# Kernel optimization log

Hardware: AMD Instinct MI355X
Metric: run time of the kernel (lower is better)

The kernel has to match this reference:

```python
import jax, jax.numpy as jnp
import numpy as np

H_HEADS = 8
DIM_HEAD = 64
NEG_BIAS = -1.0e9


def setup_inputs() -> dict:
    key = jax.random.key(0)
    ks = jax.random.split(key, 8)
    b, n, l = 4, 4096, 256
    qd, cd = 512, 768
    inner = H_HEADS * DIM_HEAD  # 512
    x = jax.random.normal(ks[0], (b, n, qd), dtype=jnp.float32)
    context = jax.random.normal(ks[1], (b, l, cd), dtype=jnp.float32)
    mask = jax.random.randint(ks[2], (b, l, 128, 128), 0, 2).astype(jnp.int32)
    Wq = jax.random.normal(ks[3], (qd, inner), dtype=jnp.float32) * 0.02
    Wk = jax.random.normal(ks[4], (cd, inner), dtype=jnp.float32) * 0.02
    Wv = jax.random.normal(ks[5], (cd, inner), dtype=jnp.float32) * 0.02
    Wo = jax.random.normal(ks[6], (inner, qd), dtype=jnp.float32) * 0.02
    bo = jnp.zeros((qd,), dtype=jnp.float32)
    return {"x": x, "context": context, "mask": mask,
            "Wq": Wq, "Wk": Wk, "Wv": Wv, "Wo": Wo, "bo": bo}


def _split_heads(t, h):
    # 'b n (h d) -> (b h) n d'
    b, n, hd = t.shape
    d = hd // h
    return t.reshape(b, n, h, d).transpose(0, 2, 1, 3).reshape(b * h, n, d)


def reference(x, context, mask, Wq, Wk, Wv, Wo, bo):
    h = H_HEADS
    scale = DIM_HEAD ** (-0.5)
    b, n, _ = x.shape
    l = context.shape[1]
    size = int(round(n ** 0.5))  # spatial side of the query grid

    q = _split_heads(x @ Wq, h)        # (b*h, n, d)
    k = _split_heads(context @ Wk, h)  # (b*h, l, d)
    v = _split_heads(context @ Wv, h)  # (b*h, l, d)

    sim = jnp.einsum('bid,bjd->bij', q, k) * scale  # (b*h, n, l)

    # F.interpolate(mask, size=size) with default 'nearest': idx = floor(i * H_in / size)
    Hin = mask.shape[2]
    idx = (jnp.arange(size) * Hin) // size
    m = mask[:, :, idx[:, None], idx[None, :]]       # (b, l, size, size)
    m = m.reshape(b, l, n).transpose(0, 2, 1)        # (b, n, l)
    m = jnp.tile(m, (h, 1, 1)).astype(bool)          # (b*h, n, l), tile order as in torch .tile(h,1,1)
    sim = jnp.where(m, sim, sim + NEG_BIAS)

    attn = jax.nn.softmax(sim, axis=-1)
    out = jnp.einsum('bij,bjd->bid', attn, v)        # (b*h, n, d)
    # '(b h) n d -> b n (h d)'
    out = out.reshape(b, h, n, DIM_HEAD).transpose(0, 2, 1, 3).reshape(b, n, h * DIM_HEAD)
    return out @ Wo + bo
```

## Files before the change

kernel.cpp:

```cpp
#include <hip/hip_runtime.h>
#include <hip/hip_bf16.h>

typedef __attribute__((ext_vector_type(8))) short short8;
typedef __attribute__((ext_vector_type(4))) float f32x4;

__device__ __forceinline__ unsigned short f2bf(float f) {
  unsigned int u = __float_as_uint(f);
  u = (u + 0x7FFFu + ((u >> 16) & 1u)) >> 16;
  return (unsigned short)u;
}

__device__ __forceinline__ unsigned int pk2(float a, float b) {
  __hip_bfloat162 h = __float22bfloat162_rn(make_float2(a, b));
  return *reinterpret_cast<unsigned int*>(&h);
}

__device__ __forceinline__ void gl_lds16(const void* g, void* l) {
  __builtin_amdgcn_global_load_lds(
      (const __attribute__((address_space(1))) void*)g,
      (__attribute__((address_space(3))) void*)l, 16, 0, 0);
}

__device__ __forceinline__ void fence_barrier() {
  asm volatile("" ::: "memory");
  __builtin_amdgcn_s_barrier();
  asm volatile("" ::: "memory");
}

__device__ __forceinline__ void store4_bf16(unsigned short* p, int stride,
                                            float v0, float v1, float v2, float v3) {
  unsigned int u01 = pk2(v0, v1), u23 = pk2(v2, v3);
  p[0] = (unsigned short)u01;
  p[stride] = (unsigned short)(u01 >> 16);
  p[2 * stride] = (unsigned short)u23;
  p[3 * stride] = (unsigned short)(u23 >> 16);
}

__global__ void prep_all(const float* __restrict__ Wq, const float* __restrict__ Wk,
                         const float* __restrict__ Wv, const float* __restrict__ Wo,
                         unsigned short* __restrict__ WqT, unsigned short* __restrict__ WkT,
                         unsigned short* __restrict__ WvT, unsigned short* __restrict__ WoT,
                         const int* __restrict__ mask, unsigned char* __restrict__ Mout,
                         const float* __restrict__ x, const float* __restrict__ ctx,
                         unsigned short* __restrict__ xb, unsigned short* __restrict__ ctxb) {
  __shared__ char smem[64 * 256];
  const int bid = blockIdx.x;
  if (bid >= 576) {
    int i = (bid - 576) * 256 + threadIdx.x;
    const float4* src;
    ushort4* dst;
    if (i < 2097152) {
      src = (const float4*)x + i;
      dst = (ushort4*)xb + i;
    } else {
      int j = i - 2097152;
      if (j >= 196608) return;
      src = (const float4*)ctx + j;
      dst = (ushort4*)ctxb + j;
    }
    float4 v = *src;
    ushort4 o;
    o.x = f2bf(v.x); o.y = f2bf(v.y); o.z = f2bf(v.z); o.w = f2bf(v.w);
    *dst = o;
    return;
  }
  if (bid < 320) {
    unsigned short(*t)[65] = (unsigned short(*)[65])smem;
    const float* W; unsigned short* WT; int K, rel;
    float scale = 1.f;
    if (bid < 64)       { W = Wq; WT = WqT; K = 512; rel = bid; scale = 0.125f * 1.4426950408889634f; }
    else if (bid < 160) { W = Wk; WT = WkT; K = 768; rel = bid - 64; }
    else if (bid < 256) { W = Wv; WT = WvT; K = 768; rel = bid - 160; }
    else                { W = Wo; WT = WoT; K = 512; rel = bid - 256; }
    const int N = 512;
    const int tk = rel >> 3, tn = rel & 7;
    const int k0 = tk * 64, n0 = tn * 64;
    const int tt = threadIdx.x;
#pragma unroll
    for (int e = 0; e < 16; ++e) {
      int idx = e * 256 + tt;
      int r = idx >> 6, c = idx & 63;
      t[r][c] = f2bf(scale * W[(size_t)(k0 + r) * N + n0 + c]);
    }
    __syncthreads();
#pragma unroll
    for (int e = 0; e < 16; ++e) {
      int idx = e * 256 + tt;
      int rr = idx & 63, cc = idx >> 6;
      WT[(size_t)(n0 + cc) * K + k0 + rr] = t[rr][cc];
    }
  } else {
    unsigned char* bits = (unsigned char*)smem;
    const int rel = bid - 320;
    const int r2g = rel & 63, bp = rel >> 6;
    const int j = threadIdx.x;
    const int4* row = (const int4*)(mask + ((size_t)(bp * 256 + j) * 128 + r2g * 2) * 128);
#pragma unroll 8
    for (int q = 0; q < 32; ++q) {
      int4 v = row[q];
      bits[(2 * q) * 256 + j] = v.x ? 1 : 0;
      bits[(2 * q + 1) * 256 + j] = v.z ? 1 : 0;
    }
    __syncthreads();
    const int t2 = threadIdx.x;
    const int c = t2 >> 2, ch = t2 & 3;
    uint4* dst = (uint4*)(Mout + ((size_t)bp * 4096 + r2g * 64 + c) * 256 + ch * 64);
#pragma unroll
    for (int q = 0; q < 4; ++q) {
      unsigned int wd[4];
#pragma unroll
      for (int wq = 0; wq < 4; ++wq) {
        unsigned int v = 0;
#pragma unroll
        for (int bb = 0; bb < 4; ++bb) {
          int ob = ch * 64 + q * 16 + wq * 4 + bb;
          int jj = ((ob & 15) << 4) | (ob >> 4);
          v |= ((unsigned int)bits[c * 256 + jj]) << (8 * bb);
        }
        wd[wq] = v;
      }
      uint4 vv; vv.x = wd[0]; vv.y = wd[1]; vv.z = wd[2]; vv.w = wd[3];
      dst[q] = vv;
    }
  }
}

__global__ __launch_bounds__(256, 2) void proj_all(
    const unsigned short* __restrict__ xb, const unsigned short* __restrict__ ctxb,
    const unsigned short* __restrict__ WqT, const unsigned short* __restrict__ WkT,
    const unsigned short* __restrict__ WvT,
    unsigned short* __restrict__ Qb, unsigned short* __restrict__ Kb,
    unsigned short* __restrict__ VTb) {
  __shared__ unsigned short lds_a[2][128 * 64];
  __shared__ unsigned short lds_b[2][128 * 64];
  const int tid = threadIdx.x;
  const int w = tid >> 6, lane = tid & 63;
  const int lo = lane & 15, hi = lane >> 4;
  const int wr = w >> 1, wc = w & 1;
  const int bid = blockIdx.x;
  const int wg = (bid & 7) * 96 + (bid >> 3);

  if (wg < 512) {
    const int m0 = (wg >> 2) * 128, n0 = (wg & 3) * 128;
    const int K = 512;
    f32x4 acc[4][4];
#pragma unroll
    for (int m = 0; m < 4; ++m)
#pragma unroll
      for (int n = 0; n < 4; ++n) acc[m][n] = (f32x4){0.f, 0.f, 0.f, 0.f};

    auto stage = [&](int buf, int k0) {
#pragma unroll
      for (int c = 0; c < 4; ++c) {
        int o = (tid + c * 256) * 16;
        int row = o >> 7, colb = (o & 127) ^ ((row & 7) << 4);
        gl_lds16((const char*)xb + ((size_t)(m0 + row) * K + k0) * 2 + colb,
                 (char*)lds_a[buf] + (w * 64 + c * 256) * 16);
      }
#pragma unroll
      for (int c = 0; c < 4; ++c) {
        int o = (tid + c * 256) * 16;
        int row = o >> 7, colb = (o & 127) ^ ((row & 7) << 4);
        gl_lds16((const char*)WqT + ((size_t)(n0 + row) * K + k0) * 2 + colb,
                 (char*)lds_b[buf] + (w * 64 + c * 256) * 16);
      }
    };

    stage(0, 0);
    int cur = 0;
    for (int t = 0; t < 8; ++t) {
      if (t < 7) {
        stage(cur ^ 1, (t + 1) * 64);
        asm volatile("s_waitcnt vmcnt(8)" ::: "memory");
      } else {
        asm volatile("s_waitcnt vmcnt(0)" ::: "memory");
      }
      fence_barrier();
      short8 a[2][4], b[2][4];
#pragma unroll
      for (int kk = 0; kk < 2; ++kk) {
#pragma unroll
        for (int m = 0; m < 4; ++m) {
          int row = wr * 64 + m * 16 + lo;
          a[kk][m] = *(const short8*)((const char*)lds_a[cur] + row * 128 +
                                      (((kk * 32 + hi * 8) * 2) ^ ((row & 7) << 4)));
        }
#pragma unroll
        for (int n = 0; n < 4; ++n) {
          int row = wc * 64 + n * 16 + lo;
          b[kk][n] = *(const short8*)((const char*)lds_b[cur] + row * 128 +
                                      (((kk * 32 + hi * 8) * 2) ^ ((row & 7) << 4)));
        }
      }
#pragma unroll
      for (int kk = 0; kk < 2; ++kk)
#pragma unroll
        for (int m = 0; m < 4; ++m)
#pragma unroll
          for (int n = 0; n < 4; ++n)
            acc[m][n] = __builtin_amdgcn_mfma_f32_16x16x32_bf16(a[kk][m], b[kk][n], acc[m][n], 0, 0, 0);
      if (t < 7) fence_barrier();
      cur ^= 1;
    }
#pragma unroll
    for (int m = 0; m < 4; ++m)
#pragma unroll
      for (int n = 0; n < 4; ++n) {
        int rbase = m0 + wr * 64 + m * 16 + hi * 4;
        int col = n0 + wc * 64 + n * 16 + lo;
        store4_bf16(&Qb[(size_t)rbase * 512 + col], 512,
                    acc[m][n][0], acc[m][n][1], acc[m][n][2], acc[m][n][3]);
      }
  } else {
    const int rel = wg - 512;
    const int z = rel >> 7, t5 = rel & 127;
    const unsigned short* BT = z ? WvT : WkT;
    const int m0 = (t5 >> 3) * 64, n0 = (t5 & 7) * 64;
    const int K = 768;
    f32x4 acc[2][2];
#pragma unroll
    for (int m = 0; m < 2; ++m)
#pragma unroll
      for (int n = 0; n < 2; ++n) acc[m][n] = (f32x4){0.f, 0.f, 0.f, 0.f};

    auto stage = [&](int buf, int k0) {
#pragma unroll
      for (int c = 0; c < 2; ++c) {
        int o = (tid + c * 256) * 16;
        int row = o >> 7, colb = (o & 127) ^ ((row & 7) << 4);
        gl_lds16((const char*)ctxb + ((size_t)(m0 + row) * K + k0) * 2 + colb,
                 (char*)lds_a[buf] + (w * 64 + c * 256) * 16);
        gl_lds16((const char*)BT + ((size_t)(n0 + row) * K + k0) * 2 + colb,
                 (char*)lds_b[buf] + (w * 64 + c * 256) * 16);
      }
    };

    stage(0, 0);
    int cur = 0;
    for (int t = 0; t < 12; ++t) {
      if (t < 11) {
        stage(cur ^ 1, (t + 1) * 64);
        asm volatile("s_waitcnt vmcnt(4)" ::: "memory");
      } else {
        asm volatile("s_waitcnt vmcnt(0)" ::: "memory");
      }
      fence_barrier();
      short8 a[2][2], b[2][2];
#pragma unroll
      for (int kk = 0; kk < 2; ++kk) {
#pragma unroll
        for (int m = 0; m < 2; ++m) {
          int row = wr * 32 + m * 16 + lo;
          a[kk][m] = *(const short8*)((const char*)lds_a[cur] + row * 128 +
                                      (((kk * 32 + hi * 8) * 2) ^ ((row & 7) << 4)));
        }
#pragma unroll
        for (int n = 0; n < 2; ++n) {
          int row = wc * 32 + n * 16 + lo;
          b[kk][n] = *(const short8*)((const char*)lds_b[cur] + row * 128 +
                                      (((kk * 32 + hi * 8) * 2) ^ ((row & 7) << 4)));
        }
      }
#pragma unroll
      for (int kk = 0; kk < 2; ++kk)
#pragma unroll
        for (int m = 0; m < 2; ++m)
#pragma unroll
          for (int n = 0; n < 2; ++n)
            acc[m][n] = __builtin_amdgcn_mfma_f32_16x16x32_bf16(a[kk][m], b[kk][n], acc[m][n], 0, 0, 0);
      if (t < 11) fence_barrier();
      cur ^= 1;
    }
#pragma unroll
    for (int m = 0; m < 2; ++m)
#pragma unroll
      for (int n = 0; n < 2; ++n) {
        int col = n0 + wc * 32 + n * 16 + lo;
        int rowg = m0 + wr * 32 + m * 16 + hi * 4;
        if (z == 0) {
          store4_bf16(&Kb[(size_t)rowg * 512 + col], 512,
                      acc[m][n][0], acc[m][n][1], acc[m][n][2], acc[m][n][3]);
        } else {
          unsigned int u01 = pk2(acc[m][n][0], acc[m][n][1]);
          unsigned int u23 = pk2(acc[m][n][2], acc[m][n][3]);
          uint2 vv; vv.x = u01; vv.y = u23;
          *(uint2*)&VTb[((size_t)(rowg >> 8) * 512 + col) * 256 + (rowg & 255)] = vv;
        }
      }
  }
}

__global__ void attn_kernel(const unsigned short* __restrict__ Qb,
                            const unsigned short* __restrict__ Kb,
                            const unsigned short* __restrict__ VTb,
                            const unsigned char* __restrict__ Mu8,
                            unsigned short* __restrict__ AOb) {
  __shared__ unsigned short kt[256 * 64];
  const int tid = threadIdx.x, w = tid >> 6, lane = tid & 63;
  const int lo = lane & 15, hi = lane >> 4;
  const int bid = blockIdx.x;
  const int wg = (bid & 7) * 256 + (bid >> 3);
  const int qt = wg & 63, h = (wg >> 6) & 7, b = wg >> 9;

#pragma unroll
  for (int c = 0; c < 8; ++c) {
    int o = (tid + c * 256) * 16;
    int j = o >> 7, colb = (o & 127) ^ ((j & 7) << 4);
    gl_lds16((const char*)Kb + ((size_t)((b * 256 + j) * 512 + h * 64)) * 2 + colb,
             (char*)kt + (w * 64 + c * 256) * 16);
  }
  short8 qf[2];
  {
    int qrow = qt * 64 + w * 16 + lo;
#pragma unroll
    for (int kk = 0; kk < 2; ++kk)
      qf[kk] = *(const short8*)&Qb[(size_t)(b * 4096 + qrow) * 512 + h * 64 + kk * 32 + hi * 8];
  }
  const unsigned char* mrow = Mu8 + ((size_t)(h & 3) * 4096 + qt * 64 + w * 16) * 256;
  uint4 mv[4];
#pragma unroll
  for (int r = 0; r < 4; ++r)
    mv[r] = *(const uint4*)(mrow + (hi * 4 + r) * 256 + lo * 16);
  __syncthreads();

  f32x4 acc[16];
#pragma unroll
  for (int nt = 0; nt < 16; ++nt) acc[nt] = (f32x4){0.f, 0.f, 0.f, 0.f};
  __builtin_amdgcn_s_setprio(1);
#pragma unroll
  for (int nt = 0; nt < 16; ++nt) {
    int j = nt * 16 + lo;
#pragma unroll
    for (int kk = 0; kk < 2; ++kk) {
      short8 bfr = *(const short8*)((const char*)kt + j * 128 +
                                    (((kk * 32 + hi * 8) * 2) ^ ((j & 7) << 4)));
      acc[nt] = __builtin_amdgcn_mfma_f32_16x16x32_bf16(qf[kk], bfr, acc[nt], 0, 0, 0);
    }
  }
  __builtin_amdgcn_s_setprio(0);

  float rsum[4] = {0.f, 0.f, 0.f, 0.f};
#pragma unroll
  for (int nt = 0; nt < 16; ++nt)
#pragma unroll
    for (int r = 0; r < 4; ++r) {
      unsigned int word = (nt < 4) ? mv[r].x : (nt < 8) ? mv[r].y : (nt < 12) ? mv[r].z : mv[r].w;
      unsigned int mbyte = (word >> ((nt & 3) * 8)) & 0xFFu;
      float p = exp2f(acc[nt][r]);
      p = mbyte ? p : 0.f;
      acc[nt][r] = p;
      rsum[r] += p;
    }
  float rinv[4];
#pragma unroll
  for (int r = 0; r < 4; ++r) {
#pragma unroll
    for (int m2 = 1; m2 < 16; m2 <<= 1)
      rsum[r] += __shfl_xor(rsum[r], m2, 64);
    rinv[r] = 1.f / rsum[r];
  }

  __syncthreads();

  {
    char* pl = (char*)kt;
    const int q0 = w * 16 + hi * 4;
    const int ro0 = (q0 + 0) * 512, sw0 = ((q0 + 0) & 7) << 4;
    const int ro1 = (q0 + 1) * 512, sw1 = ((q0 + 1) & 7) << 4;
    const int ro2 = (q0 + 2) * 512, sw2 = ((q0 + 2) & 7) << 4;
    const int ro3 = (q0 + 3) * 512, sw3 = ((q0 + 3) & 7) << 4;
#pragma unroll
    for (int nt = 0; nt < 16; ++nt) {
      int j2 = (nt * 16 + lo) * 2;
      unsigned int u01 = pk2(acc[nt][0] * rinv[0], acc[nt][1] * rinv[1]);
      unsigned int u23 = pk2(acc[nt][2] * rinv[2], acc[nt][3] * rinv[3]);
      *(unsigned short*)(pl + ro0 + (j2 ^ sw0)) = (unsigned short)u01;
      *(unsigned short*)(pl + ro1 + (j2 ^ sw1)) = (unsigned short)(u01 >> 16);
      *(unsigned short*)(pl + ro2 + (j2 ^ sw2)) = (unsigned short)u23;
      *(unsigned short*)(pl + ro3 + (j2 ^ sw3)) = (unsigned short)(u23 >> 16);
    }
  }
  __syncthreads();

  const int dh = w & 1, qh = w >> 1;
  f32x4 aco[2][2];
#pragma unroll
  for (int m = 0; m < 2; ++m)
#pragma unroll
    for (int n = 0; n < 2; ++n) aco[m][n] = (f32x4){0.f, 0.f, 0.f, 0.f};
  const size_t vbase = ((size_t)b * 512 + h * 64 + dh * 32) * 256;
#pragma unroll
  for (int ks = 0; ks < 8; ++ks) {
    short8 pa[2];
#pragma unroll
    for (int m = 0; m < 2; ++m) {
      int q = qh * 32 + m * 16 + lo;
      pa[m] = *(const short8*)((const char*)kt + q * 512 +
                               (((ks * 32 + hi * 8) * 2) ^ ((q & 7) << 4)));
    }
    __builtin_amdgcn_s_setprio(1);
#pragma unroll
    for (int n = 0; n < 2; ++n) {
      short8 vb = *(const short8*)&VTb[vbase + (size_t)(n * 16 + lo) * 256 + ks * 32 + hi * 8];
#pragma unroll
      for (int m = 0; m < 2; ++m)
        aco[m][n] = __builtin_amdgcn_mfma_f32_16x16x32_bf16(pa[m], vb, aco[m][n], 0, 0, 0);
    }
    __builtin_amdgcn_s_setprio(0);
  }

#pragma unroll
  for (int m = 0; m < 2; ++m) {
#pragma unroll
    for (int n = 0; n < 2; ++n) {
      int col = h * 64 + dh * 32 + n * 16 + lo;
      int rowg = qt * 64 + qh * 32 + m * 16 + hi * 4;
      store4_bf16(&AOb[(size_t)(b * 4096 + rowg) * 512 + col], 512,
                  aco[m][n][0], aco[m][n][1], aco[m][n][2], aco[m][n][3]);
    }
  }
}

__global__ __launch_bounds__(256, 2) void gemm_o(
    const unsigned short* __restrict__ A, const unsigned short* __restrict__ BT,
    float* __restrict__ Cout, const float* __restrict__ bias) {
  __shared__ unsigned short lds_a[2][128 * 64];
  __shared__ unsigned short lds_b[2][128 * 64];
  const int tid = threadIdx.x;
  const int w = tid >> 6, lane = tid & 63;
  const int lo = lane & 15, hi = lane >> 4;
  const int bid = blockIdx.x;
  const int wg = (bid & 7) * 64 + (bid >> 3);
  const int m0 = (wg >> 2) * 128, n0 = (wg & 3) * 128;
  const int wr = w >> 1, wc = w & 1;
  const int K = 512, N = 512;
  f32x4 acc[4][4];
#pragma unroll
  for (int m = 0; m < 4; ++m)
#pragma unroll
    for (int n = 0; n < 4; ++n) acc[m][n] = (f32x4){0.f, 0.f, 0.f, 0.f};

  auto stage = [&](int buf, int k0) {
#pragma unroll
    for (int c = 0; c < 4; ++c) {
      int o = (tid + c * 256) * 16;
      int row = o >> 7, colb = (o & 127) ^ ((row & 7) << 4);
      gl_lds16((const char*)A + ((size_t)(m0 + row) * K + k0) * 2 + colb,
               (char*)lds_a[buf] + (w * 64 + c * 256) * 16);
    }
#pragma unroll
    for (int c = 0; c < 4; ++c) {
      int o = (tid + c * 256) * 16;
      int row = o >> 7, colb = (o & 127) ^ ((row & 7) << 4);
      gl_lds16((const char*)BT + ((size_t)(n0 + row) * K + k0) * 2 + colb,
               (char*)lds_b[buf] + (w * 64 + c * 256) * 16);
    }
  };

  stage(0, 0);
  int cur = 0;
  for (int t = 0; t < 8; ++t) {
    if (t < 7) {
      stage(cur ^ 1, (t + 1) * 64);
      asm volatile("s_waitcnt vmcnt(8)" ::: "memory");
    } else {
      asm volatile("s_waitcnt vmcnt(0)" ::: "memory");
    }
    fence_barrier();
    short8 a[2][4], b[2][4];
#pragma unroll
    for (int kk = 0; kk < 2; ++kk) {
#pragma unroll
      for (int m = 0; m < 4; ++m) {
        int row = wr * 64 + m * 16 + lo;
        a[kk][m] = *(const short8*)((const char*)lds_a[cur] + row * 128 +
                                    (((kk * 32 + hi * 8) * 2) ^ ((row & 7) << 4)));
      }
#pragma unroll
      for (int n = 0; n < 4; ++n) {
        int row = wc * 64 + n * 16 + lo;
        b[kk][n] = *(const short8*)((const char*)lds_b[cur] + row * 128 +
                                    (((kk * 32 + hi * 8) * 2) ^ ((row & 7) << 4)));
      }
    }
#pragma unroll
    for (int kk = 0; kk < 2; ++kk)
#pragma unroll
      for (int m = 0; m < 4; ++m)
#pragma unroll
        for (int n = 0; n < 4; ++n)
          acc[m][n] = __builtin_amdgcn_mfma_f32_16x16x32_bf16(a[kk][m], b[kk][n], acc[m][n], 0, 0, 0);
    if (t < 7) fence_barrier();
    cur ^= 1;
  }

#pragma unroll
  for (int m = 0; m < 4; ++m)
#pragma unroll
    for (int n = 0; n < 4; ++n) {
      int rbase = m0 + wr * 64 + m * 16 + hi * 4;
      int col = n0 + wc * 64 + n * 16 + lo;
#pragma unroll
      for (int r = 0; r < 4; ++r)
        Cout[(size_t)(rbase + r) * N + col] = acc[m][n][r] + bias[col];
    }
}

extern "C" void kernel_launch(void* const* d_in, const int* in_sizes, int n_in,
                              void* d_out, int out_size, void* d_ws, size_t ws_size,
                              hipStream_t stream) {
  const float* x = (const float*)d_in[0];
  const float* ctx = (const float*)d_in[1];
  const int* mask = (const int*)d_in[2];
  const float* Wq = (const float*)d_in[3];
  const float* Wk = (const float*)d_in[4];
  const float* Wv = (const float*)d_in[5];
  const float* Wo = (const float*)d_in[6];
  const float* bo = (const float*)d_in[7];
  float* out = (float*)d_out;

  char* ws = (char*)d_ws;
  size_t off = 0;
  auto alloc = [&](size_t bytes) {
    char* p = ws + off;
    off += (bytes + 255) & ~(size_t)255;
    return p;
  };
  unsigned short* xb   = (unsigned short*)alloc((size_t)16384 * 512 * 2);
  unsigned short* ctxb = (unsigned short*)alloc((size_t)1024 * 768 * 2);
  unsigned short* WqT  = (unsigned short*)alloc((size_t)512 * 512 * 2);
  unsigned short* WkT  = (unsigned short*)alloc((size_t)512 * 768 * 2);
  unsigned short* WvT  = (unsigned short*)alloc((size_t)512 * 768 * 2);
  unsigned short* WoT  = (unsigned short*)alloc((size_t)512 * 512 * 2);
  unsigned short* Qb   = (unsigned short*)alloc((size_t)16384 * 512 * 2);
  unsigned short* Kb   = (unsigned short*)alloc((size_t)1024 * 512 * 2);
  unsigned short* VTb  = (unsigned short*)alloc((size_t)4 * 512 * 256 * 2);
  unsigned short* AOb  = (unsigned short*)alloc((size_t)16384 * 512 * 2);
  unsigned char*  Mu8  = (unsigned char*)alloc((size_t)4 * 4096 * 256);

  prep_all<<<9536, 256, 0, stream>>>(Wq, Wk, Wv, Wo, WqT, WkT, WvT, WoT, mask, Mu8, x, ctx, xb, ctxb);
  proj_all<<<768, 256, 0, stream>>>(xb, ctxb, WqT, WkT, WvT, Qb, Kb, VTb);
  attn_kernel<<<2048, 256, 0, stream>>>(Qb, Kb, VTb, Mu8, AOb);
  gemm_o<<<512, 256, 0, stream>>>(AOb, WoT, out, bo);
}
```

Before: 81.02 us.

## Fuse x fp32-to-bf16 conversion into Q projection GEMM A-operand staging

Removes the separate pass that converts x (16384x512 fp32) into a bf16 workspace buffer. The Q projection GEMM now loads fp32 x through registers, packs it to bf16 and writes it into swizzled LDS, with the loads for the next k-tile overlapped with the MFMA work on the current one. This saves a full write and re-read of the bf16 copy of x. In exchange the A operand uses register-staged loads instead of direct global-to-LDS copies, which adds register pressure and VALU packing work inside the GEMM loop.

```diff
diff --git a/kernel.cpp b/kernel.cpp
--- a/kernel.cpp
+++ b/kernel.cpp
@@ -41,27 +41,16 @@
                          unsigned short* __restrict__ WqT, unsigned short* __restrict__ WkT,
                          unsigned short* __restrict__ WvT, unsigned short* __restrict__ WoT,
                          const int* __restrict__ mask, unsigned char* __restrict__ Mout,
-                         const float* __restrict__ x, const float* __restrict__ ctx,
-                         unsigned short* __restrict__ xb, unsigned short* __restrict__ ctxb) {
+                         const float* __restrict__ ctx, unsigned short* __restrict__ ctxb) {
   __shared__ char smem[64 * 256];
   const int bid = blockIdx.x;
   if (bid >= 576) {
     int i = (bid - 576) * 256 + threadIdx.x;
-    const float4* src;
-    ushort4* dst;
-    if (i < 2097152) {
-      src = (const float4*)x + i;
-      dst = (ushort4*)xb + i;
-    } else {
-      int j = i - 2097152;
-      if (j >= 196608) return;
-      src = (const float4*)ctx + j;
-      dst = (ushort4*)ctxb + j;
-    }
-    float4 v = *src;
+    if (i >= 196608) return;
+    float4 v = ((const float4*)ctx)[i];
     ushort4 o;
     o.x = f2bf(v.x); o.y = f2bf(v.y); o.z = f2bf(v.z); o.w = f2bf(v.w);
-    *dst = o;
+    ((ushort4*)ctxb)[i] = o;
     return;
   }
   if (bid < 320) {
@@ -126,7 +115,7 @@
 }
 
 __global__ __launch_bounds__(256, 2) void proj_all(
-    const unsigned short* __restrict__ xb, const unsigned short* __restrict__ ctxb,
+    const float* __restrict__ x, const unsigned short* __restrict__ ctxb,
     const unsigned short* __restrict__ WqT, const unsigned short* __restrict__ WkT,
     const unsigned short* __restrict__ WvT,
     unsigned short* __restrict__ Qb, unsigned short* __restrict__ Kb,
@@ -143,20 +132,31 @@
   if (wg < 512) {
     const int m0 = (wg >> 2) * 128, n0 = (wg & 3) * 128;
     const int K = 512;
+    const int arow = tid >> 4, acol = tid & 15;
     f32x4 acc[4][4];
 #pragma unroll
     for (int m = 0; m < 4; ++m)
 #pragma unroll
       for (int n = 0; n < 4; ++n) acc[m][n] = (f32x4){0.f, 0.f, 0.f, 0.f};
 
-    auto stage = [&](int buf, int k0) {
-#pragma unroll
-      for (int c = 0; c < 4; ++c) {
-        int o = (tid + c * 256) * 16;
-        int row = o >> 7, colb = (o & 127) ^ ((row & 7) << 4);
-        gl_lds16((const char*)xb + ((size_t)(m0 + row) * K + k0) * 2 + colb,
-                 (char*)lds_a[buf] + (w * 64 + c * 256) * 16);
-      }
+    float4 areg[8];
+    auto loadA = [&](int k0) {
+#pragma unroll
+      for (int p = 0; p < 8; ++p)
+        areg[p] = *(const float4*)&x[(size_t)(m0 + p * 16 + arow) * K + k0 + acol * 4];
+    };
+    auto writeA = [&](int buf) {
+#pragma unroll
+      for (int p = 0; p < 8; ++p) {
+        int row = p * 16 + arow;
+        uint2 vv;
+        vv.x = pk2(areg[p].x, areg[p].y);
+        vv.y = pk2(areg[p].z, areg[p].w);
+        int boff = (row * 128 + acol * 8) ^ ((row & 7) << 4);
+        *(uint2*)((char*)lds_a[buf] + boff) = vv;
+      }
+    };
+    auto stageB = [&](int buf, int k0) {
 #pragma unroll
       for (int c = 0; c < 4; ++c) {
         int o = (tid + c * 256) * 16;
@@ -166,16 +166,19 @@
       }
     };
 
-    stage(0, 0);
+    loadA(0);
+    stageB(0, 0);
+    asm volatile("s_waitcnt vmcnt(4)" ::: "memory");
+    writeA(0);
+    asm volatile("s_waitcnt vmcnt(0) lgkmcnt(0)" ::: "memory");
+    __builtin_amdgcn_s_barrier();
+
     int cur = 0;
     for (int t = 0; t < 8; ++t) {
       if (t < 7) {
-        stage(cur ^ 1, (t + 1) * 64);
-        asm volatile("s_waitcnt vmcnt(8)" ::: "memory");
-      } else {
-        asm volatile("s_waitcnt vmcnt(0)" ::: "memory");
-      }
-      fence_barrier();
+        loadA((t + 1) * 64);
+        stageB(cur ^ 1, (t + 1) * 64);
+      }
       short8 a[2][4], b[2][4];
 #pragma unroll
       for (int kk = 0; kk < 2; ++kk) {
@@ -199,7 +202,12 @@
 #pragma unroll
           for (int n = 0; n < 4; ++n)
             acc[m][n] = __builtin_amdgcn_mfma_f32_16x16x32_bf16(a[kk][m], b[kk][n], acc[m][n], 0, 0, 0);
-      if (t < 7) fence_barrier();
+      if (t < 7) {
+        asm volatile("s_waitcnt vmcnt(4)" ::: "memory");
+        writeA(cur ^ 1);
+      }
+      asm volatile("s_waitcnt vmcnt(0) lgkmcnt(0)" ::: "memory");
+      __builtin_amdgcn_s_barrier();
       cur ^= 1;
     }
 #pragma unroll
@@ -526,7 +534,6 @@
     off += (bytes + 255) & ~(size_t)255;
     return p;
   };
-  unsigned short* xb   = (unsigned short*)alloc((size_t)16384 * 512 * 2);
   unsigned short* ctxb = (unsigned short*)alloc((size_t)1024 * 768 * 2);
   unsigned short* WqT  = (unsigned short*)alloc((size_t)512 * 512 * 2);
   unsigned short* WkT  = (unsigned short*)alloc((size_t)512 * 768 * 2);
@@ -538,8 +545,8 @@
   unsigned short* AOb  = (unsigned short*)alloc((size_t)16384 * 512 * 2);
   unsigned char*  Mu8  = (unsigned char*)alloc((size_t)4 * 4096 * 256);
 
-  prep_all<<<9536, 256, 0, stream>>>(Wq, Wk, Wv, Wo, WqT, WkT, WvT, WoT, mask, Mu8, x, ctx, xb, ctxb);
-  proj_all<<<768, 256, 0, stream>>>(xb, ctxb, WqT, WkT, WvT, Qb, Kb, VTb);
+  prep_all<<<1344, 256, 0, stream>>>(Wq, Wk, Wv, Wo, WqT, WkT, WvT, WoT, mask, Mu8, ctx, ctxb);
+  proj_all<<<768, 256, 0, stream>>>(x, ctxb, WqT, WkT, WvT, Qb, Kb, VTb);
   attn_kernel<<<2048, 256, 0, stream>>>(Qb, Kb, VTb, Mu8, AOb);
   gemm_o<<<512, 256, 0, stream>>>(AOb, WoT, out, bo);
 }
```

After: 88.04 us. +8.7%, slower.
